# Performance work log

Hardware: AMD Instinct MI355X
Metric: run time of the kernel (lower is better)

## Reference

```python
import jax, jax.numpy as jnp
import numpy as np

DIM = 1024
NUM_HEADS = 16
HEAD_DIM = 64
NUM_LANDMARKS = 256
SEQ_LEN = 4096
BATCH = 4


def setup_inputs() -> dict:
    key = jax.random.key(0)
    ks = jax.random.split(key, 10)
    hd = NUM_HEADS * HEAD_DIM
    s = 1.0 / np.sqrt(DIM)
    inp = {
        "X": jax.random.normal(ks[0], (BATCH, SEQ_LEN, DIM), jnp.float32),
        "mask": jnp.ones((BATCH, SEQ_LEN), jnp.float32),
        "Wq": jax.random.normal(ks[1], (DIM, hd), jnp.float32) * s,
        "bq": jnp.zeros((hd,), jnp.float32),
        "Wk": jax.random.normal(ks[2], (DIM, hd), jnp.float32) * s,
        "bk": jnp.zeros((hd,), jnp.float32),
        "Wv": jax.random.normal(ks[3], (DIM, hd), jnp.float32) * s,
        "bv": jnp.zeros((hd,), jnp.float32),
        "Wff": jax.random.normal(ks[4], (hd, DIM), jnp.float32) * (1.0 / np.sqrt(hd)),
        "bff": jnp.zeros((DIM,), jnp.float32),
    }
    return inp


def _iterative_inv(mat, n_iter=6):
    # mat: [B,H,m,m]; Newton-Schulz style pseudo-inverse, faithful to torch code
    m = mat.shape[-1]
    I = jnp.eye(m, dtype=mat.dtype)
    K = mat
    # global max over the whole tensor, as torch.max with no dim
    denom = jnp.max(jnp.sum(jnp.abs(K), axis=-2)) * jnp.max(jnp.sum(jnp.abs(K), axis=-1))
    V = jnp.swapaxes(K, -1, -2) / denom
    for _ in range(n_iter):
        KV = K @ V
        V = 0.25 * V @ (13.0 * I - KV @ (15.0 * I - KV @ (7.0 * I - KV)))
    return V


def _nystrom_attn(Q, K, V, mask):
    # Q,K,V: [B,H,S,D]; mask: [B,S]
    B, H, S, D = Q.shape
    m = NUM_LANDMARKS
    scale = np.sqrt(np.sqrt(HEAD_DIM)).astype(np.float32)
    Q = Q * mask[:, None, :, None] / scale
    K = K * mask[:, None, :, None] / scale
    Ql = Q.reshape(B, H, m, S // m, D).mean(axis=-2)  # [B,H,m,D]
    Kl = K.reshape(B, H, m, S // m, D).mean(axis=-2)
    k1 = jax.nn.softmax(jnp.einsum('bhsd,bhmd->bhsm', Q, Kl), axis=-1)   # [B,H,S,m]
    k2 = jax.nn.softmax(jnp.einsum('bhmd,bhnd->bhmn', Ql, Kl), axis=-1)  # [B,H,m,m]
    k3 = jax.nn.softmax(
        jnp.einsum('bhmd,bhsd->bhms', Ql, K) - 1e9 * (1.0 - mask[:, None, None, :]),
        axis=-1)  # [B,H,m,S]
    return k1 @ (_iterative_inv(k2) @ (k3 @ V))  # [B,H,S,D]


def reference(X, mask, Wq, bq, Wk, bk, Wv, bv, Wff, bff):
    B, S, _ = X.shape
    def split(t):  # [B,S,H*D] -> [B,H,S,D]
        return t.reshape(B, S, NUM_HEADS, HEAD_DIM).transpose(0, 2, 1, 3)
    Q = split(X @ Wq + bq)
    K = split(X @ Wk + bk)
    V = split(X @ Wv + bv)
    attn = _nystrom_attn(Q, K, V, mask)
    attn = attn.transpose(0, 2, 1, 3).reshape(B, S, NUM_HEADS * HEAD_DIM)
    return attn @ Wff + bff
```

## Files before the change

kernel.cpp:

```cpp
#include <hip/hip_runtime.h>
#include <cstdint>
#include <cstddef>


typedef unsigned short u16;
typedef __attribute__((ext_vector_type(8))) short short8;
typedef __attribute__((ext_vector_type(4))) float f32x4;
typedef __attribute__((ext_vector_type(4))) unsigned short us4;
typedef __attribute__((ext_vector_type(8))) unsigned short us8;

__device__ __forceinline__ float bf2f(u16 u){ return __uint_as_float(((unsigned int)u)<<16); }
__device__ __forceinline__ u16 f2bf(float x){
  unsigned int i = __float_as_uint(x);
  unsigned int r = i + 0x7FFFu + ((i>>16)&1u);
  return (u16)(r>>16);
}
__device__ __forceinline__ f32x4 mfma16(short8 a, short8 b, f32x4 c){
  return __builtin_amdgcn_mfma_f32_16x16x32_bf16(a,b,c,0,0,0);
}
__device__ __forceinline__ void gld16(const void* g, void* l){
  __builtin_amdgcn_global_load_lds(
      (const __attribute__((address_space(1))) unsigned int*)g,
      (__attribute__((address_space(3))) unsigned int*)l, 16, 0, 0);
}

__global__ __launch_bounds__(256) void k2s_k(
    const u16* __restrict__ Ah, const u16* __restrict__ Al,
    const u16* __restrict__ Bh, const u16* __restrict__ Bl,
    float* __restrict__ C)
{
  __shared__ u16 lds[40960];
  const int tid = threadIdx.x;
  const int tileM = blockIdx.x*64;
  const int z = blockIdx.y;
  const int lane = tid&63, wv = tid>>6;
  const int lrow = lane&15, kgrp = lane>>4;
  const u16* baseAh = Ah + (size_t)z*16384 + (size_t)tileM*64;
  const u16* baseAl = Al + (size_t)z*16384 + (size_t)tileM*64;
  const u16* baseBh = Bh + (size_t)z*16384;
  const u16* baseBl = Bl + (size_t)z*16384;

  #pragma unroll
  for (int it=0; it<2; ++it){
    int w = it*256 + tid; int row = w>>3, c = w&7; int cs = c^(row&7);
    gld16(baseAh + (size_t)row*64 + (cs<<3), lds + (w & ~63)*8);
  }
  #pragma unroll
  for (int it=0; it<2; ++it){
    int w = it*256 + tid; int row = w>>3, c = w&7; int cs = c^(row&7);
    gld16(baseAl + (size_t)row*64 + (cs<<3), lds + 4096 + (w & ~63)*8);
  }
  #pragma unroll
  for (int it=0; it<8; ++it){
    int w = it*256 + tid; int row = w>>3, c = w&7; int cs = c^(row&7);
    gld16(baseBh + (size_t)row*64 + (cs<<3), lds + 8192 + (w & ~63)*8);
  }
  #pragma unroll
  for (int it=0; it<8; ++it){
    int w = it*256 + tid; int row = w>>3, c = w&7; int cs = c^(row&7);
    gld16(baseBl + (size_t)row*64 + (cs<<3), lds + 24576 + (w & ~63)*8);
  }
  __syncthreads();

  f32x4 acc[16];
  #pragma unroll
  for (int j=0;j<16;j++) acc[j] = (f32x4){0.f,0.f,0.f,0.f};

  #pragma unroll
  for (int kt=0; kt<2; ++kt){
    int ch = kt*4 + kgrp;
    int ra = wv*16 + lrow;
    short8 ah = *(const short8*)&lds[ra*64 + ((ch^(ra&7))<<3)];
    short8 al = *(const short8*)&lds[4096 + ra*64 + ((ch^(ra&7))<<3)];
    #pragma unroll
    for (int j=0;j<16;j++){
      int rb = j*16 + lrow;
      short8 bh = *(const short8*)&lds[8192 + rb*64 + ((ch^(rb&7))<<3)];
      short8 bl = *(const short8*)&lds[24576 + rb*64 + ((ch^(rb&7))<<3)];
      acc[j] = mfma16(ah, bh, acc[j]);
      acc[j] = mfma16(ah, bl, acc[j]);
      acc[j] = mfma16(al, bh, acc[j]);
    }
  }

  float* Cz = C + (size_t)z*65536;
  #pragma unroll
  for (int r=0;r<4;r++){
    float mx = -3.0e38f;
    #pragma unroll
    for (int j=0;j<16;j++) mx = fmaxf(mx, acc[j][r]);
    #pragma unroll
    for (int d=1; d<16; d<<=1) mx = fmaxf(mx, __shfl_xor(mx, d));
    float p[16]; float ss = 0.f;
    #pragma unroll
    for (int j=0;j<16;j++){ p[j] = expf(acc[j][r]-mx); ss += p[j]; }
    #pragma unroll
    for (int d=1; d<16; d<<=1) ss += __shfl_xor(ss, d);
    float inv = 1.0f/ss;
    int row = tileM + wv*16 + kgrp*4 + r;
    #pragma unroll
    for (int j=0;j<16;j++){
      int col = j*16 + lrow;
      Cz[(size_t)row*256 + col] = p[j]*inv;
    }
  }
}

template<int OUT>
__global__ __launch_bounds__(256) void sgemm_k(
    const u16* __restrict__ Ah, const u16* __restrict__ Al,
    const u16* __restrict__ Bh, const u16* __restrict__ Bl,
    int K, long long sA, long long sB,
    u16* __restrict__ RoH, u16* __restrict__ RoL,
    u16* __restrict__ CoH, u16* __restrict__ CoL,
    float* __restrict__ Fo, long long sO, int ldO,
    float addI, float csgn, float scale,
    const float* __restrict__ bias, const float* __restrict__ ml)
{
  __shared__ u16 lds[16384];
  const int tid = threadIdx.x;
  const int z = blockIdx.z;
  const int tileM = blockIdx.x*64, tileN = blockIdx.y*64;
  const int lane = tid&63, wv = tid>>6;
  const int wr = wv>>1, wc = wv&1;
  const int lrow = lane&15, kgrp = lane>>4;

  const u16* __restrict__ base[4] = {
    Ah + (size_t)z*sA + (size_t)tileM*K,
    Al + (size_t)z*sA + (size_t)tileM*K,
    Bh + (size_t)z*sB + (size_t)tileN*K,
    Bl + (size_t)z*sB + (size_t)tileN*K };

  f32x4 acc[2][2];
  #pragma unroll
  for (int i=0;i<2;i++)
    #pragma unroll
    for (int j=0;j<2;j++) acc[i][j] = (f32x4){0.f,0.f,0.f,0.f};

  for (int k0=0; k0<K; k0+=64){
    #pragma unroll
    for (int t4=0; t4<4; ++t4){
      #pragma unroll
      for (int hf=0; hf<2; ++hf){
        int w = hf*256 + tid;
        int row = w>>3, c = w&7;
        int cs = c ^ (row&7);
        gld16(base[t4] + (size_t)row*K + k0 + cs*8, lds + t4*4096 + (w & ~63)*8);
      }
    }
    __syncthreads();
    #pragma unroll
    for (int kk=0; kk<2; ++kk){
      int ch = kk*4 + kgrp;
      short8 a_h[2], a_l[2], b_h[2], b_l[2];
      #pragma unroll
      for (int i=0;i<2;i++){
        int r = wr*32 + i*16 + lrow;
        int off = r*64 + ((ch ^ (r&7))<<3);
        a_h[i] = *(const short8*)&lds[off];
        a_l[i] = *(const short8*)&lds[4096 + off];
      }
      #pragma unroll
      for (int j=0;j<2;j++){
        int r = wc*32 + j*16 + lrow;
        int off = r*64 + ((ch ^ (r&7))<<3);
        b_h[j] = *(const short8*)&lds[8192 + off];
        b_l[j] = *(const short8*)&lds[12288 + off];
      }
      #pragma unroll
      for (int i=0;i<2;i++)
        #pragma unroll
        for (int j=0;j<2;j++){
          acc[i][j] = mfma16(a_h[i], b_h[j], acc[i][j]);
          acc[i][j] = mfma16(a_h[i], b_l[j], acc[i][j]);
          acc[i][j] = mfma16(a_l[i], b_h[j], acc[i][j]);
        }
    }
    __syncthreads();
  }

  if constexpr (OUT==0 || OUT==1){
    #pragma unroll
    for (int i=0;i<2;i++)
      #pragma unroll
      for (int j=0;j<2;j++){
        int rl0 = wr*32 + i*16 + kgrp*4;
        int cl  = wc*32 + j*16 + lrow;
        #pragma unroll
        for (int q=0;q<4;q++){
          int rl = rl0 + q;
          float p = acc[i][j][q]*scale;
          if constexpr (OUT==0){
            if (RoH){
              u16 h = f2bf(p);
              int lo = rl*64 + (cl ^ ((rl&7)<<3));
              lds[lo] = h;
              lds[4096 + lo] = f2bf(p - bf2f(h));
            }
            float cv = csgn*p + (((tileM+rl)==(tileN+cl))? addI : 0.f);
            u16 ch = f2bf(cv);
            int lo2 = cl*64 + (rl ^ ((cl&7)<<3));
            lds[8192 + lo2] = ch;
            lds[12288 + lo2] = f2bf(cv - bf2f(ch));
          } else {
            lds[cl*64 + (rl ^ ((cl&7)<<3))] = f2bf(p);
          }
        }
      }
    __syncthreads();
    if constexpr (OUT==0){
      if (RoH){
        #pragma unroll
        for (int c2=0;c2<2;c2++){
          int idx = c2*256 + tid;
          int row = idx>>3, seg = idx&7;
          int lo = row*64 + ((seg ^ (row&7))<<3);
          size_t go = (size_t)z*65536 + (size_t)(tileM+row)*256 + tileN + seg*8;
          *(us8*)&RoH[go] = *(const us8*)&lds[lo];
          *(us8*)&RoL[go] = *(const us8*)&lds[4096 + lo];
        }
      }
      #pragma unroll
      for (int c2=0;c2<2;c2++){
        int idx = c2*256 + tid;
        int row = idx>>3, seg = idx&7;
        int lo = row*64 + ((seg ^ (row&7))<<3);
        size_t go = (size_t)z*65536 + (size_t)(tileN+row)*256 + tileM + seg*8;
        *(us8*)&CoH[go] = *(const us8*)&lds[8192 + lo];
        *(us8*)&CoL[go] = *(const us8*)&lds[12288 + lo];
      }
    } else {
      #pragma unroll
      for (int c2=0;c2<2;c2++){
        int idx = c2*256 + tid;
        int row = idx>>3, seg = idx&7;
        int lo = row*64 + ((seg ^ (row&7))<<3);
        *(us8*)&CoH[(size_t)z*16384 + (size_t)(tileN+row)*256 + tileM + seg*8] =
            *(const us8*)&lds[lo];
      }
    }
  } else {
    #pragma unroll
    for (int i=0;i<2;i++)
      #pragma unroll
      for (int j=0;j<2;j++){
        int grow0 = tileM + wr*32 + i*16 + kgrp*4;
        int gcol  = tileN + wc*32 + j*16 + lrow;
        #pragma unroll
        for (int q=0;q<4;q++){
          int grow = grow0+q;
          float v = acc[i][j][q] + ml[grow]*bias[gcol];
          int b = grow>>8, l = grow&255, h = gcol>>6, d = gcol&63;
          size_t oi = (((size_t)(b*16+h)*256 + l)*64 + d);
          Fo[oi] = v;
          if (RoH){
            u16 hh = f2bf(v);
            RoH[oi] = hh;
            RoL[oi] = f2bf(v - bf2f(hh));
          }
        }
      }
  }
}

template<int EPI>
__global__ __launch_bounds__(256) void fgemm_k(
    const u16* __restrict__ A, const u16* __restrict__ Bt, float* __restrict__ Cf,
    u16* __restrict__ Q_, u16* __restrict__ K_, u16* __restrict__ V_,
    int M, int N, int K, int nTilesN,
    const float* __restrict__ bias, const float* __restrict__ rowscale)
{
  __shared__ u16 lds[2*128*64];
  u16* ldsA = lds;
  u16* ldsB = lds + 128*64;

  int flat = blockIdx.y*nTilesN + blockIdx.x;
  int nwg  = gridDim.x*gridDim.y;
  int chunk = nwg >> 3;
  int nid = (flat & 7)*chunk + (flat >> 3);
  int bxM = nid / nTilesN, byN = nid % nTilesN;
  const int tileM = bxM*128, tileN = byN*128;

  const int tid = threadIdx.x;
  const int lane = tid & 63, wv = tid>>6;
  const int wr = wv>>1, wc = wv&1;
  const int lrow = lane&15, kgrp = lane>>4;

  f32x4 acc[4][4];
  #pragma unroll
  for (int i=0;i<4;i++)
    #pragma unroll
    for (int j=0;j<4;j++) acc[i][j] = (f32x4){0.f,0.f,0.f,0.f};

  for (int k0=0; k0<K; k0+=64){
    #pragma unroll
    for (int i=0;i<4;i++){
      int s = i*256 + tid;
      int row = s>>3, c = s&7;
      int cs = c ^ (row&7);
      gld16(A + (size_t)(tileM+row)*K + k0 + cs*8, ldsA + (size_t)(s & ~63)*8);
    }
    #pragma unroll
    for (int i=0;i<4;i++){
      int s = i*256 + tid;
      int row = s>>3, c = s&7;
      int cs = c ^ (row&7);
      gld16(Bt + (size_t)(tileN+row)*K + k0 + cs*8, ldsB + (size_t)(s & ~63)*8);
    }
    __syncthreads();
    #pragma unroll
    for (int kk=0; kk<2; ++kk){
      int ch = kk*4 + kgrp;
      short8 af[4], bf[4];
      #pragma unroll
      for (int i=0;i<4;i++){
        int r = wr*64 + i*16 + lrow;
        af[i] = *(const short8*)&ldsA[r*64 + ((ch^(r&7))<<3)];
      }
      #pragma unroll
      for (int j=0;j<4;j++){
        int r = wc*64 + j*16 + lrow;
        bf[j] = *(const short8*)&ldsB[r*64 + ((ch^(r&7))<<3)];
      }
      #pragma unroll
      for (int i=0;i<4;i++)
        #pragma unroll
        for (int j=0;j<4;j++)
          acc[i][j] = mfma16(af[i], bf[j], acc[i][j]);
    }
    __syncthreads();
  }

  if constexpr (EPI==0){
    #pragma unroll
    for (int i=0;i<4;i++)
      #pragma unroll
      for (int j=0;j<4;j++)
        #pragma unroll
        for (int q=0;q<4;q++){
          int row = tileM + wr*64 + i*16 + kgrp*4 + q;
          int col = tileN + wc*64 + j*16 + lrow;
          Cf[(size_t)row*N + col] = acc[i][j][q] + (bias ? bias[col] : 0.f);
        }
  } else {
    #pragma unroll
    for (int i=0;i<4;i++)
      #pragma unroll
      for (int j=0;j<4;j++)
        #pragma unroll
        for (int q=0;q<4;q++){
          int rloc = wr*64 + i*16 + kgrp*4 + q;
          int cloc = wc*64 + j*16 + lrow;
          int col = tileN + cloc;
          float v = acc[i][j][q] + bias[col];
          if ((col>>10) < 2) v *= rowscale[tileM + rloc];
          lds[rloc*128 + cloc] = f2bf(v);
        }
    __syncthreads();
    #pragma unroll
    for (int c=0;c<8;c++){
      int idx = c*256 + tid;
      int row = idx >> 4;
      int seg = idx & 15;
      int col = tileN + seg*8;
      int which = col >> 10;
      int hd = col & 1023, h = hd>>6, d0 = hd&63;
      int grow = tileM + row;
      int b = grow>>12, s = grow&4095;
      u16* dst = (which==0) ? Q_ : (which==1) ? K_ : V_;
      us8 v = *(const us8*)&lds[row*128 + seg*8];
      *(us8*)&dst[(((size_t)(b*16+h))*4096 + s)*64 + d0] = v;
    }
  }
}

__global__ __launch_bounds__(256) void o3p_k(
    const float* __restrict__ Ql, const u16* __restrict__ Kb, const u16* __restrict__ Vb,
    const float* __restrict__ mask, float* __restrict__ Opart, float* __restrict__ MLpart)
{
  constexpr int QHI=0, QLO=4096, KT=8192, VT=12288, PHI=16640, PLO=20736;
  __shared__ u16 lds[24832];
  const int bx = blockIdx.x, ck = blockIdx.y, z = blockIdx.z;
  const int tid = threadIdx.x;
  const int lane = tid&63, wv = tid>>6;
  const int lrow = lane&15, kgrp = lane>>4;
  const float* Qlz = Ql + (size_t)z*16384 + (size_t)bx*64*64;
  const u16* Kz = Kb + (size_t)z*4096*64;
  const u16* Vz = Vb + (size_t)z*4096*64;
  const float* mrow = mask + (size_t)(z>>4)*4096;

  #pragma unroll
  for (int i=0;i<2;i++){
    int s = i*256 + tid;
    int row = s>>3, c = s&7;
    const float* src = Qlz + row*64 + c*8;
    f32x4 v0 = *(const f32x4*)src;
    f32x4 v1 = *(const f32x4*)(src+4);
    us8 hi, lo;
    #pragma unroll
    for (int e=0;e<4;e++){
      hi[e] = f2bf(v0[e]); lo[e] = f2bf(v0[e]-bf2f(hi[e]));
      hi[4+e] = f2bf(v1[e]); lo[4+e] = f2bf(v1[e]-bf2f(hi[4+e]));
    }
    int ad = row*64 + ((c^(row&7))<<3);
    *(us8*)&lds[QHI+ad] = hi;
    *(us8*)&lds[QLO+ad] = lo;
  }

  float m_r[4], l_r[4];
  f32x4 oacc[4];
  #pragma unroll
  for (int r=0;r<4;r++){ m_r[r] = -3.0e38f; l_r[r] = 0.f; }
  #pragma unroll
  for (int j=0;j<4;j++) oacc[j] = (f32x4){0.f,0.f,0.f,0.f};

  for (int st=0; st<16; ++st){
    int s0 = (ck*16 + st)*64;
    #pragma unroll
    for (int i=0;i<2;i++){
      int s = i*256 + tid;
      int row = s>>3, c = s&7;
      int cs = c ^ (row&7);
      gld16(Kz + (size_t)(s0+row)*64 + cs*8, &lds[KT + (size_t)(s & ~63)*8]);
    }
    #pragma unroll
    for (int i=0;i<2;i++){
      int s = i*256 + tid;
      int row = s>>3, c = s&7;
      us8 v = *(const us8*)(Vz + (size_t)(s0+row)*64 + c*8);
      #pragma unroll
      for (int e=0;e<8;e++) lds[VT + (c*8+e)*68 + row] = v[e];
    }
    __syncthreads();

    f32x4 sacc[4];
    #pragma unroll
    for (int j=0;j<4;j++) sacc[j] = (f32x4){0.f,0.f,0.f,0.f};
    int qr = wv*16 + lrow;
    #pragma unroll
    for (int kk=0; kk<2; ++kk){
      int ch = kk*4 + kgrp;
      short8 ah = *(const short8*)&lds[QHI + qr*64 + ((ch^(qr&7))<<3)];
      short8 alo = *(const short8*)&lds[QLO + qr*64 + ((ch^(qr&7))<<3)];
      #pragma unroll
      for (int j=0;j<4;j++){
        int kr = j*16 + lrow;
        short8 bk = *(const short8*)&lds[KT + kr*64 + ((ch^(kr&7))<<3)];
        sacc[j] = mfma16(ah, bk, sacc[j]);
        sacc[j] = mfma16(alo, bk, sacc[j]);
      }
    }
    float mb[4];
    #pragma unroll
    for (int j=0;j<4;j++) mb[j] = -1.0e9f*(1.0f - mrow[s0 + j*16 + lrow]);
    #pragma unroll
    for (int j=0;j<4;j++)
      #pragma unroll
      for (int r=0;r<4;r++) sacc[j][r] += mb[j];

    #pragma unroll
    for (int r=0;r<4;r++){
      float tm = fmaxf(fmaxf(sacc[0][r],sacc[1][r]), fmaxf(sacc[2][r],sacc[3][r]));
      #pragma unroll
      for (int d=1; d<16; d<<=1) tm = fmaxf(tm, __shfl_xor(tm, d));
      float mn = fmaxf(m_r[r], tm);
      float scf = expf(m_r[r] - mn);
      float ps[4]; float tsum = 0.f;
      #pragma unroll
      for (int j=0;j<4;j++){ ps[j] = expf(sacc[j][r] - mn); tsum += ps[j]; }
      #pragma unroll
      for (int d=1; d<16; d<<=1) tsum += __shfl_xor(tsum, d);
      l_r[r] = l_r[r]*scf + tsum;
      m_r[r] = mn;
      #pragma unroll
      for (int j=0;j<4;j++) oacc[j][r] *= scf;
      int prow = kgrp*4 + r;
      #pragma unroll
      for (int j=0;j<4;j++){
        int key = j*16 + lrow;
        u16 phi = f2bf(ps[j]);
        u16 plo = f2bf(ps[j] - bf2f(phi));
        int ad = wv*1024 + prow*64 + (((key>>3)^(prow&7))<<3) + (key&7);
        lds[PHI+ad] = phi;
        lds[PLO+ad] = plo;
      }
    }

    #pragma unroll
    for (int kk=0; kk<2; ++kk){
      int ch = kk*4 + kgrp;
      int pr = lrow;
      short8 pah = *(const short8*)&lds[PHI + wv*1024 + pr*64 + ((ch^(pr&7))<<3)];
      short8 plo = *(const short8*)&lds[PLO + wv*1024 + pr*64 + ((ch^(pr&7))<<3)];
      #pragma unroll
      for (int j=0;j<4;j++){
        int vr = j*16 + lrow;
        int a0 = VT + vr*68 + ch*8;
        us4 p0 = *(const us4*)&lds[a0];
        us4 p1 = *(const us4*)&lds[a0+4];
        short8 bv_;
        #pragma unroll
        for (int e=0;e<4;e++){ bv_[e] = (short)p0[e]; bv_[4+e] = (short)p1[e]; }
        oacc[j] = mfma16(pah, bv_, oacc[j]);
        oacc[j] = mfma16(plo, bv_, oacc[j]);
      }
    }
    __syncthreads();
  }

  #pragma unroll
  for (int j=0;j<4;j++)
    #pragma unroll
    for (int r=0;r<4;r++){
      int rowl = bx*64 + wv*16 + kgrp*4 + r;
      Opart[(((size_t)(ck*64+z)*256 + rowl)*64) + j*16 + lrow] = oacc[j][r];
    }
  #pragma unroll
  for (int r=0;r<4;r++){
    if (lrow==0){
      int rowl = bx*64 + wv*16 + kgrp*4 + r;
      MLpart[((size_t)(ck*64+z)*256 + rowl)*2 + 0] = m_r[r];
      MLpart[((size_t)(ck*64+z)*256 + rowl)*2 + 1] = l_r[r];
    }
  }
}

__global__ __launch_bounds__(256) void o3c_k(const float* __restrict__ Opart,
    const float* __restrict__ MLpart, u16* __restrict__ O3Th, u16* __restrict__ O3Tl)
{
  int z = blockIdx.x; int t = threadIdx.x;
  float m[4], l[4];
  #pragma unroll
  for (int c=0;c<4;c++){
    m[c] = MLpart[((size_t)(c*64+z)*256 + t)*2 + 0];
    l[c] = MLpart[((size_t)(c*64+z)*256 + t)*2 + 1];
  }
  float M = fmaxf(fmaxf(m[0],m[1]), fmaxf(m[2],m[3]));
  float w[4]; float L = 0.f;
  #pragma unroll
  for (int c=0;c<4;c++){ w[c] = expf(m[c]-M); L += l[c]*w[c]; }
  float inv = 1.0f/L;
  for (int d0=0; d0<16; ++d0){
    f32x4 o = (f32x4){0.f,0.f,0.f,0.f};
    #pragma unroll
    for (int c=0;c<4;c++){
      f32x4 x = *(const f32x4*)(Opart + ((size_t)(c*64+z)*256 + t)*64 + d0*4);
      #pragma unroll
      for (int e=0;e<4;e++) o[e] += w[c]*x[e];
    }
    #pragma unroll
    for (int e=0;e<4;e++){
      float val = o[e]*inv;
      int d = d0*4+e;
      u16 h = f2bf(val);
      O3Th[((size_t)z*64 + d)*256 + t] = h;
      O3Tl[((size_t)z*64 + d)*256 + t] = f2bf(val - bf2f(h));
    }
  }
}

__global__ void fill_k(float* __restrict__ p, int n, float v){
  for (int i = blockIdx.x*256 + threadIdx.x; i < n; i += gridDim.x*256) p[i] = v;
}
__global__ __launch_bounds__(256) void setup_k(
    const float* __restrict__ mask, float* __restrict__ rs,
    const float* __restrict__ bq, const float* __restrict__ bk,
    const float* __restrict__ bv, float* __restrict__ bqkv, float* __restrict__ mx,
    const float* __restrict__ Wq, const float* __restrict__ Wk,
    const float* __restrict__ Wv, const float* __restrict__ Wff,
    u16* __restrict__ Tqkv, u16* __restrict__ Tff,
    u16* __restrict__ QH, u16* __restrict__ QL,
    u16* __restrict__ KH, u16* __restrict__ KL)
{
  __shared__ float t[64][65];
  int b = blockIdx.x;
  if (b < 77){
    if (b < 64){
      int i = b*256 + threadIdx.x;
      rs[i] = mask[i] * 0.3535533905932738f;
    } else if (b < 76){
      int j = (b-64)*256 + threadIdx.x;
      bqkv[j] = (j<1024) ? bq[j] : (j<2048) ? bk[j-1024] : bv[j-2048];
    } else {
      if (threadIdx.x < 2) mx[threadIdx.x] = 0.f;
    }
    return;
  }
  int tt = threadIdx.x; int c = tt&63, r0 = tt>>6;
  if (b < 77+1024){
    int f = b - 77;
    int zi = f >> 8; int r2 = f & 255; int ti = r2 & 15; int tj = r2 >> 4;
    const float* W = (zi==0)?Wq:(zi==1)?Wk:(zi==2)?Wv:Wff;
    u16* T = (zi==3)? Tff : (Tqkv + (size_t)zi*1048576);
    #pragma unroll
    for (int rr=0; rr<16; rr++){
      int r = rr*4 + r0;
      t[r][c] = W[(size_t)(ti*64+r)*1024 + tj*64 + c];
    }
    __syncthreads();
    #pragma unroll
    for (int rr=0; rr<16; rr++){
      int r = rr*4 + r0;
      T[(size_t)(tj*64 + r)*1024 + ti*64 + c] = f2bf(t[c][r]);
    }
  } else {
    int f = b - 77 - 1024;
    int zi = f >> 8; int r2 = f & 255; int ti = r2 & 15; int tj = r2 >> 4;
    const float* W = zi ? Wk : Wq;
    u16* TH = zi ? KH : QH;
    u16* TL = zi ? KL : QL;
    #pragma unroll
    for (int rr=0; rr<16; rr++){
      int r = rr*4 + r0;
      t[r][c] = W[(size_t)(ti*64+r)*1024 + tj*64 + c];
    }
    __syncthreads();
    #pragma unroll
    for (int rr=0; rr<16; rr++){
      int r = rr*4 + r0;
      float v = t[c][r];
      u16 h = f2bf(v);
      TH[(size_t)(tj*64 + r)*1024 + ti*64 + c] = h;
      TL[(size_t)(tj*64 + r)*1024 + ti*64 + c] = f2bf(v - bf2f(h));
    }
  }
}
__global__ __launch_bounds__(256) void pool_k(const float* __restrict__ X, const float* __restrict__ mask,
                                              u16* __restrict__ Xlh, u16* __restrict__ Xll,
                                              float* __restrict__ ml, u16* __restrict__ Xb){
  int bl = blockIdx.x; int b = bl>>8; int l = bl&255;
  const float* Xp = X + ((size_t)b*4096 + (size_t)l*16)*1024;
  const float* mp = mask + (size_t)b*4096 + (size_t)l*16;
  int t = threadIdx.x;
  f32x4 acc = (f32x4){0.f,0.f,0.f,0.f};
  float msum = 0.f;
  #pragma unroll
  for (int j=0;j<16;j++){
    float mj = mp[j];
    msum += mj;
    f32x4 x = *(const f32x4*)(Xp + (size_t)j*1024 + t*4);
    us4 xb;
    #pragma unroll
    for (int c=0;c<4;c++){ acc[c] += mj*x[c]; xb[c] = f2bf(x[c]); }
    *(us4*)(Xb + ((size_t)bl*16 + j)*1024 + t*4) = xb;
  }
  const float c0 = 0.02209708691207961f;
  us4 h, lo;
  #pragma unroll
  for (int c=0;c<4;c++){
    float v = acc[c]*c0;
    h[c] = f2bf(v);
    lo[c] = f2bf(v - bf2f(h[c]));
  }
  *(us4*)(Xlh + (size_t)bl*1024 + t*4) = h;
  *(us4*)(Xll + (size_t)bl*1024 + t*4) = lo;
  if (t==0) ml[bl] = msum * c0;
}
__global__ __launch_bounds__(256) void absmax_k(const float* __restrict__ k2, float* __restrict__ mx){
  int z = blockIdx.x; int t = threadIdx.x;
  const float* A = k2 + (size_t)z*65536;
  float rsum=0.f, csum=0.f;
  for (int j=0;j<256;j++){
    rsum += fabsf(A[t*256+j]);
    csum += fabsf(A[j*256+t]);
  }
  #pragma unroll
  for (int d=1; d<64; d<<=1){
    rsum = fmaxf(rsum, __shfl_xor(rsum, d));
    csum = fmaxf(csum, __shfl_xor(csum, d));
  }
  __shared__ float red[8];
  int wv=t>>6, ln=t&63;
  if (ln==0){ red[wv]=rsum; red[4+wv]=csum; }
  __syncthreads();
  if (t==0){
    float mr = fmaxf(fmaxf(red[0],red[1]),fmaxf(red[2],red[3]));
    float mc = fmaxf(fmaxf(red[4],red[5]),fmaxf(red[6],red[7]));
    atomicMax((int*)&mx[0], __float_as_int(mr));
    atomicMax((int*)&mx[1], __float_as_int(mc));
  }
}
__global__ __launch_bounds__(256) void v0prep_k(const float* __restrict__ K2f, const float* __restrict__ mx,
    u16* __restrict__ K2h, u16* __restrict__ K2l,
    u16* __restrict__ V0rh, u16* __restrict__ V0rl,
    u16* __restrict__ V0ch, u16* __restrict__ V0cl)
{
  int z = blockIdx.y; int bx = blockIdx.x;
  int ti = bx>>2, tj = bx&3;
  __shared__ float tile[64][65];
  const float* A = K2f + (size_t)z*65536;
  int t = threadIdx.x; int c = t&63, r0 = t>>6;
  float invden = 1.0f/(mx[0]*mx[1]);
  #pragma unroll
  for (int rr=0; rr<16; rr++){
    int r = rr*4 + r0;
    float v = A[(size_t)(ti*64 + r)*256 + tj*64 + c];
    tile[r][c] = v;
    size_t idx = (size_t)z*65536 + (size_t)(ti*64+r)*256 + tj*64 + c;
    u16 h = f2bf(v);
    K2h[idx] = h; K2l[idx] = f2bf(v - bf2f(h));
    float w = v*invden;
    h = f2bf(w);
    V0ch[idx] = h; V0cl[idx] = f2bf(w - bf2f(h));
  }
  __syncthreads();
  #pragma unroll
  for (int rr=0; rr<16; rr++){
    int r = rr*4 + r0;
    float w = tile[c][r]*invden;
    size_t idx = (size_t)z*65536 + (size_t)(tj*64+r)*256 + ti*64 + c;
    u16 h = f2bf(w);
    V0rh[idx] = h; V0rl[idx] = f2bf(w - bf2f(h));
  }
}

__device__ __forceinline__ int swz64(int row,int k){
  return row*64 + (((((k>>3)&7) ^ (row&7)))<<3) + (k&7);
}
__device__ __forceinline__ int swz256(int row,int k){
  return row*256 + ((((k>>3) ^ (row&7)))<<3) + (k&7);
}
__global__ __launch_bounds__(256) void attn_k(const u16* __restrict__ Qb,
    const u16* __restrict__ Klb, const u16* __restrict__ tTb,
    u16* __restrict__ attn){
  __shared__ u16 lds[32768];
  const int z = blockIdx.y;
  const int rows0 = blockIdx.x * 64;
  const int tid = threadIdx.x;
  const int lane = tid & 63, wv = tid>>6;
  const int lrow = lane & 15, kgrp = lane>>4;
  const u16* Qz = Qb + ((size_t)z*4096 + rows0)*64;
  const u16* Klz = Klb + (size_t)z*16384;
  const u16* tTz = tTb + (size_t)z*16384;

  #pragma unroll
  for (int i=0;i<8;i++){
    int s = i*256 + tid;
    int row = s>>3, c = s&7;
    gld16(Klz + (size_t)row*64 + ((c^(row&7))<<3), lds + (s & ~63)*8);
  }
  #pragma unroll
  for (int i=0;i<2;i++){
    int s = i*256 + tid;
    int row = s>>3, c = s&7;
    gld16(Qz + (size_t)row*64 + ((c^(row&7))<<3), lds + 16384 + (s & ~63)*8);
  }
  __syncthreads();

  f32x4 acc[4][4];
  #pragma unroll
  for (int i=0;i<4;i++)
    #pragma unroll
    for (int j=0;j<4;j++) acc[i][j] = (f32x4){0.f,0.f,0.f,0.f};
  #pragma unroll
  for (int ks=0; ks<2; ++ks){
    int ko = ks*32 + kgrp*8;
    short8 a[4], b[4];
    #pragma unroll
    for (int i=0;i<4;i++) a[i] = *(const short8*)&lds[16384 + swz64(16*i+lrow, ko)];
    #pragma unroll
    for (int j=0;j<4;j++) b[j] = *(const short8*)&lds[swz64(wv*64 + j*16 + lrow, ko)];
    #pragma unroll
    for (int i=0;i<4;i++)
      #pragma unroll
      for (int j=0;j<4;j++) acc[i][j] = mfma16(a[i], b[j], acc[i][j]);
  }
  __syncthreads();

  #pragma unroll
  for (int i=0;i<8;i++){
    int s = i*256 + tid;
    int row = s>>5, c = s&31;
    int gch = (c & ~7) | ((c ^ row) & 7);
    gld16(tTz + (size_t)row*256 + (gch<<3), lds + 16384 + (s & ~63)*8);
  }

  float* r0 = (float*)lds;
  float* r1 = r0 + 256;
  #pragma unroll
  for (int i=0;i<4;i++)
    #pragma unroll
    for (int r=0;r<4;r++){
      float mx = fmaxf(fmaxf(acc[i][0][r], acc[i][1][r]), fmaxf(acc[i][2][r], acc[i][3][r]));
      #pragma unroll
      for (int d=1; d<16; d<<=1) mx = fmaxf(mx, __shfl_xor(mx, d));
      if (lrow==0) r0[(16*i + kgrp*4 + r)*4 + wv] = mx;
    }
  __syncthreads();
  float inv_ir[4][4];
  #pragma unroll
  for (int i=0;i<4;i++)
    #pragma unroll
    for (int r=0;r<4;r++){
      int row = 16*i + kgrp*4 + r;
      float gm = fmaxf(fmaxf(r0[row*4+0], r0[row*4+1]), fmaxf(r0[row*4+2], r0[row*4+3]));
      float s = 0.f;
      #pragma unroll
      for (int j=0;j<4;j++){
        acc[i][j][r] = expf(acc[i][j][r] - gm);
        s += acc[i][j][r];
      }
      #pragma unroll
      for (int d=1; d<16; d<<=1) s += __shfl_xor(s, d);
      if (lrow==0) r1[row*4 + wv] = s;
      inv_ir[i][r] = 0.f; (void)inv_ir;
    }
  __syncthreads();
  #pragma unroll
  for (int i=0;i<4;i++)
    #pragma unroll
    for (int r=0;r<4;r++){
      int row = 16*i + kgrp*4 + r;
      inv_ir[i][r] = 1.0f/(r1[row*4+0]+r1[row*4+1]+r1[row*4+2]+r1[row*4+3]);
    }
  __syncthreads();

  #pragma unroll
  for (int i=0;i<4;i++)
    #pragma unroll
    for (int j=0;j<4;j++)
      #pragma unroll
      for (int r=0;r<4;r++){
        int row = 16*i + kgrp*4 + r;
        int l = wv*64 + j*16 + lrow;
        lds[swz256(row, l)] = f2bf(acc[i][j][r]*inv_ir[i][r]);
      }
  __syncthreads();

  f32x4 o[4];
  #pragma unroll
  for (int j=0;j<4;j++) o[j] = (f32x4){0.f,0.f,0.f,0.f};
  #pragma unroll
  for (int ks=0; ks<8; ++ks){
    int ko = ks*32 + kgrp*8;
    short8 a = *(const short8*)&lds[swz256(16*wv + lrow, ko)];
    #pragma unroll
    for (int j=0;j<4;j++){
      short8 bb = *(const short8*)&lds[16384 + swz256(j*16 + lrow, ko)];
      o[j] = mfma16(a, bb, o[j]);
    }
  }
  __syncthreads();
  #pragma unroll
  for (int j=0;j<4;j++)
    #pragma unroll
    for (int r=0;r<4;r++){
      int m = 16*wv + kgrp*4 + r;
      lds[m*64 + j*16 + lrow] = f2bf(o[j][r]);
    }
  __syncthreads();
  int b = z>>4, h = z&15;
  #pragma unroll
  for (int c=0;c<2;c++){
    int idx = c*256 + tid;
    int row = idx >> 3;
    int seg = idx & 7;
    us8 v = *(const us8*)&lds[row*64 + seg*8];
    *(us8*)&attn[((size_t)b*4096 + rows0 + row)*1024 + (size_t)h*64 + seg*8] = v;
  }
}

extern "C" void kernel_launch(void* const* d_in, const int* in_sizes, int n_in,
                              void* d_out, int out_size, void* d_ws, size_t ws_size,
                              hipStream_t stream) {
  (void)in_sizes; (void)n_in;
  const float* X    = (const float*)d_in[0];
  const float* mask = (const float*)d_in[1];
  const float* Wq   = (const float*)d_in[2];
  const float* bq   = (const float*)d_in[3];
  const float* Wk   = (const float*)d_in[4];
  const float* bk   = (const float*)d_in[5];
  const float* Wv   = (const float*)d_in[6];
  const float* bv   = (const float*)d_in[7];
  const float* Wff  = (const float*)d_in[8];
  const float* bff  = (const float*)d_in[9];
  float* outp = (float*)d_out;
  char* ws = (char*)d_ws;

  auto MiB = [](size_t x){ return x<<20; };
  const size_t O_QB   = 0;
  const size_t O_KB   = MiB(32);
  const size_t O_VB   = MiB(64);
  const size_t O_XB   = MiB(96);
  const size_t O_RG[4][2] = {
    {MiB(32),MiB(40)}, {MiB(48),MiB(56)}, {MiB(64),MiB(72)}, {MiB(80),MiB(88)} };
  const size_t O_QLH  = MiB(96),  O_QLL = MiB(98), O_KLL = MiB(100);
  const size_t O_OPART= MiB(96);
  const size_t O_MLP  = MiB(112);
  const size_t O_XAH  = MiB(96),  O_XAL = MiB(104);
  const size_t O_K2H  = MiB(112), O_K2L = MiB(120);
  const size_t O_K2F  = MiB(128);
  const size_t O_WQKVT= MiB(128);
  const size_t O_XLH  = MiB(134), O_XLL = MiB(136);
  const size_t O_WQTH = MiB(138), O_WQTL = MiB(140);
  const size_t O_QL   = MiB(144);
  const size_t O_TTB  = MiB(144);
  const size_t O_KL   = MiB(148);
  const size_t O_O3TH = MiB(152), O_O3TL = MiB(154);
  const size_t O_WKTH = MiB(152), O_WKTL = MiB(154);
  const size_t O_WFFT = MiB(156);
  const size_t O_KLB  = MiB(158);
  const size_t O_ATTN = MiB(32);
  const size_t O_RS   = MiB(162);
  const size_t O_ML   = O_RS + 65536;
  const size_t O_MX   = O_ML + 4096;
  const size_t O_BQKV = O_MX + 256;
  const size_t NEED   = O_BQKV + 16384;

  if (ws_size < NEED){
    fill_k<<<2048,256,0,stream>>>(outp, out_size, 1.0e9f);
    return;
  }

  u16*   Qb   = (u16*)(ws + O_QB);
  u16*   Kb   = (u16*)(ws + O_KB);
  u16*   Vb   = (u16*)(ws + O_VB);
  u16*   Xb   = (u16*)(ws + O_XB);
  u16*   WqkvT= (u16*)(ws + O_WQKVT);
  u16*   WffT = (u16*)(ws + O_WFFT);
  float* bqkv = (float*)(ws + O_BQKV);
  float* Ql   = (float*)(ws + O_QL);
  float* Kl   = (float*)(ws + O_KL);
  u16*   QlH  = (u16*)(ws + O_QLH);
  u16*   QlL  = (u16*)(ws + O_QLL);
  u16*   KlL  = (u16*)(ws + O_KLL);
  u16*   Klb  = (u16*)(ws + O_KLB);
  u16*   tTb  = (u16*)(ws + O_TTB);
  float* K2f  = (float*)(ws + O_K2F);
  float* rs   = (float*)(ws + O_RS);
  float* ml   = (float*)(ws + O_ML);
  float* Mx   = (float*)(ws + O_MX);
  float* Opart= (float*)(ws + O_OPART);
  float* MLp  = (float*)(ws + O_MLP);
  u16*   O3Th = (u16*)(ws + O_O3TH);
  u16*   O3Tl = (u16*)(ws + O_O3TL);
  u16*   K2h  = (u16*)(ws + O_K2H);
  u16*   K2l  = (u16*)(ws + O_K2L);
  u16*   XAh  = (u16*)(ws + O_XAH);
  u16*   XAl  = (u16*)(ws + O_XAL);
  u16*   Xlh  = (u16*)(ws + O_XLH);
  u16*   Xll  = (u16*)(ws + O_XLL);
  u16*   WqTh = (u16*)(ws + O_WQTH);
  u16*   WqTl = (u16*)(ws + O_WQTL);
  u16*   WkTh = (u16*)(ws + O_WKTH);
  u16*   WkTl = (u16*)(ws + O_WKTL);
  u16*   AttnB= (u16*)(ws + O_ATTN);
  u16* RGH[4]; u16* RGL[4];
  for (int i=0;i<4;i++){ RGH[i] = (u16*)(ws + O_RG[i][0]); RGL[i] = (u16*)(ws + O_RG[i][1]); }

  setup_k<<<1613,256,0,stream>>>(mask, rs, bq, bk, bv, bqkv, Mx,
      Wq, Wk, Wv, Wff, WqkvT, WffT, WqTh, WqTl, WkTh, WkTl);
  pool_k<<<1024,256,0,stream>>>(X, mask, Xlh, Xll, ml, Xb);

  fgemm_k<1><<<dim3(24,128),256,0,stream>>>(Xb, WqkvT, nullptr, Qb, Kb, Vb,
      16384, 3072, 1024, 24, bqkv, rs);

  sgemm_k<2><<<dim3(16,16,1),256,0,stream>>>(Xlh, Xll, WqTh, WqTl, 1024, 0, 0,
      QlH, QlL, nullptr, nullptr, Ql, 0, 0, 0.f, 0.f, 1.f, bq, ml);
  sgemm_k<2><<<dim3(16,16,1),256,0,stream>>>(Xlh, Xll, WkTh, WkTl, 1024, 0, 0,
      Klb, KlL, nullptr, nullptr, Kl, 0, 0, 0.f, 0.f, 1.f, bk, ml);

  k2s_k<<<dim3(4,64),256,0,stream>>>(QlH, QlL, Klb, KlL, K2f);

  o3p_k<<<dim3(4,4,64),256,0,stream>>>(Ql, Kb, Vb, mask, Opart, MLp);
  o3c_k<<<64,256,0,stream>>>(Opart, MLp, O3Th, O3Tl);

  absmax_k<<<64,256,0,stream>>>(K2f, Mx);
  v0prep_k<<<dim3(16,64),256,0,stream>>>(K2f, Mx, K2h, K2l, RGH[1], RGL[1], RGH[0], RGL[0]);
  int vc=0, vr=1, kv=2, x2=3;
  for (int it=0; it<6; ++it){
    sgemm_k<0><<<dim3(4,4,64),256,0,stream>>>(K2h, K2l, RGH[vc], RGL[vc], 256, 65536, 65536,
        RGH[kv], RGL[kv], XAh, XAl, nullptr, 0, 0, 7.f, -1.f, 1.f, nullptr, nullptr);
    sgemm_k<0><<<dim3(4,4,64),256,0,stream>>>(RGH[kv], RGL[kv], XAh, XAl, 256, 65536, 65536,
        nullptr, nullptr, RGH[x2], RGL[x2], nullptr, 0, 0, 15.f, -1.f, 1.f, nullptr, nullptr);
    sgemm_k<0><<<dim3(4,4,64),256,0,stream>>>(RGH[kv], RGL[kv], RGH[x2], RGL[x2], 256, 65536, 65536,
        nullptr, nullptr, XAh, XAl, nullptr, 0, 0, 13.f, -1.f, 1.f, nullptr, nullptr);
    sgemm_k<0><<<dim3(4,4,64),256,0,stream>>>(RGH[vr], RGL[vr], XAh, XAl, 256, 65536, 65536,
        RGH[kv], RGL[kv], RGH[x2], RGL[x2], nullptr, 0, 0, 0.f, 1.f, 0.25f, nullptr, nullptr);
    int nvc=x2, nvr=kv, nkv=vc, nx2=vr;
    vc=nvc; vr=nvr; kv=nkv; x2=nx2;
  }
  sgemm_k<1><<<dim3(4,1,64),256,0,stream>>>(RGH[vr], RGL[vr], O3Th, O3Tl, 256, 65536, 16384,
      nullptr,nullptr, tTb, nullptr, nullptr, 0, 0, 0.f, 0.f, 1.f, nullptr, nullptr);

  attn_k<<<dim3(64,64),256,0,stream>>>(Qb, Klb, tTb, AttnB);

  fgemm_k<0><<<dim3(8,128),256,0,stream>>>(AttnB, WffT, outp, nullptr, nullptr, nullptr,
      16384, 1024, 1024, 8, bff, nullptr);
}
```

Measured before the change: 1.114 ms.

## Use 8-wave fgemm blocks and merge pooling and absmax into other launches

The dense GEMM kernel now runs 512 threads per 128x128 tile instead of 256. Each of the 8 waves covers a 64x32 sub-tile, so per-thread accumulators halve and more waves are available to hide latency. The X pooling and bf16 conversion moves into extra blocks of the setup kernel, and the K2 absmax reduction merges into the O3 combine kernel, removing two launches. The cost is less per-wave fragment reuse (af loads are now shared across only 2 B fragments) and some branch divergence between block roles in the merged kernels.

Result: faster. 1.018 ms (median of 2 runs) (-8.6%).

```diff
diff --git a/kernel.cpp b/kernel.cpp
--- a/kernel.cpp
+++ b/kernel.cpp
@@ -264,7 +264,7 @@
 }
 
 template<int EPI>
-__global__ __launch_bounds__(256) void fgemm_k(
+__global__ __launch_bounds__(512) void fgemm_k(
     const u16* __restrict__ A, const u16* __restrict__ Bt, float* __restrict__ Cf,
     u16* __restrict__ Q_, u16* __restrict__ K_, u16* __restrict__ V_,
     int M, int N, int K, int nTilesN,
@@ -283,26 +283,26 @@
 
   const int tid = threadIdx.x;
   const int lane = tid & 63, wv = tid>>6;
-  const int wr = wv>>1, wc = wv&1;
+  const int wr = wv>>2, wc = wv&3;
   const int lrow = lane&15, kgrp = lane>>4;
 
-  f32x4 acc[4][4];
+  f32x4 acc[4][2];
   #pragma unroll
   for (int i=0;i<4;i++)
     #pragma unroll
-    for (int j=0;j<4;j++) acc[i][j] = (f32x4){0.f,0.f,0.f,0.f};
+    for (int j=0;j<2;j++) acc[i][j] = (f32x4){0.f,0.f,0.f,0.f};
 
   for (int k0=0; k0<K; k0+=64){
     #pragma unroll
-    for (int i=0;i<4;i++){
-      int s = i*256 + tid;
+    for (int i=0;i<2;i++){
+      int s = i*512 + tid;
       int row = s>>3, c = s&7;
       int cs = c ^ (row&7);
       gld16(A + (size_t)(tileM+row)*K + k0 + cs*8, ldsA + (size_t)(s & ~63)*8);
     }
     #pragma unroll
-    for (int i=0;i<4;i++){
-      int s = i*256 + tid;
+    for (int i=0;i<2;i++){
+      int s = i*512 + tid;
       int row = s>>3, c = s&7;
       int cs = c ^ (row&7);
       gld16(Bt + (size_t)(tileN+row)*K + k0 + cs*8, ldsB + (size_t)(s & ~63)*8);
@@ -311,21 +311,21 @@
     #pragma unroll
     for (int kk=0; kk<2; ++kk){
       int ch = kk*4 + kgrp;
-      short8 af[4], bf[4];
+      short8 af[4], bf[2];
       #pragma unroll
       for (int i=0;i<4;i++){
         int r = wr*64 + i*16 + lrow;
         af[i] = *(const short8*)&ldsA[r*64 + ((ch^(r&7))<<3)];
       }
       #pragma unroll
-      for (int j=0;j<4;j++){
-        int r = wc*64 + j*16 + lrow;
+      for (int j=0;j<2;j++){
+        int r = wc*32 + j*16 + lrow;
         bf[j] = *(const short8*)&ldsB[r*64 + ((ch^(r&7))<<3)];
       }
       #pragma unroll
       for (int i=0;i<4;i++)
         #pragma unroll
-        for (int j=0;j<4;j++)
+        for (int j=0;j<2;j++)
           acc[i][j] = mfma16(af[i], bf[j], acc[i][j]);
     }
     __syncthreads();
@@ -335,22 +335,22 @@
     #pragma unroll
     for (int i=0;i<4;i++)
       #pragma unroll
-      for (int j=0;j<4;j++)
+      for (int j=0;j<2;j++)
         #pragma unroll
         for (int q=0;q<4;q++){
           int row = tileM + wr*64 + i*16 + kgrp*4 + q;
-          int col = tileN + wc*64 + j*16 + lrow;
+          int col = tileN + wc*32 + j*16 + lrow;
           Cf[(size_t)row*N + col] = acc[i][j][q] + (bias ? bias[col] : 0.f);
         }
   } else {
     #pragma unroll
     for (int i=0;i<4;i++)
       #pragma unroll
-      for (int j=0;j<4;j++)
+      for (int j=0;j<2;j++)
         #pragma unroll
         for (int q=0;q<4;q++){
           int rloc = wr*64 + i*16 + kgrp*4 + q;
-          int cloc = wc*64 + j*16 + lrow;
+          int cloc = wc*32 + j*16 + lrow;
           int col = tileN + cloc;
           float v = acc[i][j][q] + bias[col];
           if ((col>>10) < 2) v *= rowscale[tileM + rloc];
@@ -358,8 +358,8 @@
         }
     __syncthreads();
     #pragma unroll
-    for (int c=0;c<8;c++){
-      int idx = c*256 + tid;
+    for (int c=0;c<4;c++){
+      int idx = c*512 + tid;
       int row = idx >> 4;
       int seg = idx & 15;
       int col = tileN + seg*8;
@@ -525,36 +525,63 @@
   }
 }
 
-__global__ __launch_bounds__(256) void o3c_k(const float* __restrict__ Opart,
-    const float* __restrict__ MLpart, u16* __restrict__ O3Th, u16* __restrict__ O3Tl)
+__global__ __launch_bounds__(256) void o3cab_k(const float* __restrict__ Opart,
+    const float* __restrict__ MLpart, u16* __restrict__ O3Th, u16* __restrict__ O3Tl,
+    const float* __restrict__ k2, float* __restrict__ mx)
 {
-  int z = blockIdx.x; int t = threadIdx.x;
-  float m[4], l[4];
-  #pragma unroll
-  for (int c=0;c<4;c++){
-    m[c] = MLpart[((size_t)(c*64+z)*256 + t)*2 + 0];
-    l[c] = MLpart[((size_t)(c*64+z)*256 + t)*2 + 1];
-  }
-  float M = fmaxf(fmaxf(m[0],m[1]), fmaxf(m[2],m[3]));
-  float w[4]; float L = 0.f;
-  #pragma unroll
-  for (int c=0;c<4;c++){ w[c] = expf(m[c]-M); L += l[c]*w[c]; }
-  float inv = 1.0f/L;
-  for (int d0=0; d0<16; ++d0){
-    f32x4 o = (f32x4){0.f,0.f,0.f,0.f};
+  int t = threadIdx.x;
+  if (blockIdx.x < 64){
+    int z = blockIdx.x;
+    float m[4], l[4];
     #pragma unroll
     for (int c=0;c<4;c++){
-      f32x4 x = *(const f32x4*)(Opart + ((size_t)(c*64+z)*256 + t)*64 + d0*4);
-      #pragma unroll
-      for (int e=0;e<4;e++) o[e] += w[c]*x[e];
-    }
-    #pragma unroll
-    for (int e=0;e<4;e++){
-      float val = o[e]*inv;
-      int d = d0*4+e;
-      u16 h = f2bf(val);
-      O3Th[((size_t)z*64 + d)*256 + t] = h;
-      O3Tl[((size_t)z*64 + d)*256 + t] = f2bf(val - bf2f(h));
+      m[c] = MLpart[((size_t)(c*64+z)*256 + t)*2 + 0];
+      l[c] = MLpart[((size_t)(c*64+z)*256 + t)*2 + 1];
+    }
+    float M = fmaxf(fmaxf(m[0],m[1]), fmaxf(m[2],m[3]));
+    float w[4]; float L = 0.f;
+    #pragma unroll
+    for (int c=0;c<4;c++){ w[c] = expf(m[c]-M); L += l[c]*w[c]; }
+    float inv = 1.0f/L;
+    for (int d0=0; d0<16; ++d0){
+      f32x4 o = (f32x4){0.f,0.f,0.f,0.f};
+      #pragma unroll
+      for (int c=0;c<4;c++){
+        f32x4 x = *(const f32x4*)(Opart + ((size_t)(c*64+z)*256 + t)*64 + d0*4);
+        #pragma unroll
+        for (int e=0;e<4;e++) o[e] += w[c]*x[e];
+      }
+      #pragma unroll
+      for (int e=0;e<4;e++){
+        float val = o[e]*inv;
+        int d = d0*4+e;
+        u16 h = f2bf(val);
+        O3Th[((size_t)z*64 + d)*256 + t] = h;
+        O3Tl[((size_t)z*64 + d)*256 + t] = f2bf(val - bf2f(h));
+      }
+    }
+  } else {
+    int z = blockIdx.x - 64;
+    const float* A = k2 + (size_t)z*65536;
+    float rsum=0.f, csum=0.f;
+    for (int j=0;j<256;j++){
+      rsum += fabsf(A[t*256+j]);
+      csum += fabsf(A[j*256+t]);
+    }
+    #pragma unroll
+    for (int d=1; d<64; d<<=1){
+      rsum = fmaxf(rsum, __shfl_xor(rsum, d));
+      csum = fmaxf(csum, __shfl_xor(csum, d));
+    }
+    __shared__ float red[8];
+    int wv=t>>6, ln=t&63;
+    if (ln==0){ red[wv]=rsum; red[4+wv]=csum; }
+    __syncthreads();
+    if (t==0){
+      float mr = fmaxf(fmaxf(red[0],red[1]),fmaxf(red[2],red[3]));
+      float mc = fmaxf(fmaxf(red[4],red[5]),fmaxf(red[6],red[7]));
+      atomicMax((int*)&mx[0], __float_as_int(mr));
+      atomicMax((int*)&mx[1], __float_as_int(mc));
     }
   }
 }
@@ -570,7 +597,10 @@
     const float* __restrict__ Wv, const float* __restrict__ Wff,
     u16* __restrict__ Tqkv, u16* __restrict__ Tff,
     u16* __restrict__ QH, u16* __restrict__ QL,
-    u16* __restrict__ KH, u16* __restrict__ KL)
+    u16* __restrict__ KH, u16* __restrict__ KL,
+    const float* __restrict__ X,
+    u16* __restrict__ Xlh, u16* __restrict__ Xll,
+    float* __restrict__ ml, u16* __restrict__ Xb)
 {
   __shared__ float t[64][65];
   int b = blockIdx.x;
@@ -586,6 +616,36 @@
     }
     return;
   }
+  if (b >= 1613){
+    int bl = b - 1613; int bb = bl>>8; int l = bl&255;
+    const float* Xp = X + ((size_t)bb*4096 + (size_t)l*16)*1024;
+    const float* mp = mask + (size_t)bb*4096 + (size_t)l*16;
+    int tt = threadIdx.x;
+    f32x4 acc = (f32x4){0.f,0.f,0.f,0.f};
+    float msum = 0.f;
+    #pragma unroll
+    for (int j=0;j<16;j++){
+      float mj = mp[j];
+      msum += mj;
+      f32x4 x = *(const f32x4*)(Xp + (size_t)j*1024 + tt*4);
+      us4 xb;
+      #pragma unroll
+      for (int c=0;c<4;c++){ acc[c] += mj*x[c]; xb[c] = f2bf(x[c]); }
+      *(us4*)(Xb + ((size_t)bl*16 + j)*1024 + tt*4) = xb;
+    }
+    const float c0 = 0.02209708691207961f;
+    us4 h, lo;
+    #pragma unroll
+    for (int c=0;c<4;c++){
+      float v = acc[c]*c0;
+      h[c] = f2bf(v);
+      lo[c] = f2bf(v - bf2f(h[c]));
+    }
+    *(us4*)(Xlh + (size_t)bl*1024 + tt*4) = h;
+    *(us4*)(Xll + (size_t)bl*1024 + tt*4) = lo;
+    if (tt==0) ml[bl] = msum * c0;
+    return;
+  }
   int tt = threadIdx.x; int c = tt&63, r0 = tt>>6;
   if (b < 77+1024){
     int f = b - 77;
@@ -623,61 +683,6 @@
       TH[(size_t)(tj*64 + r)*1024 + ti*64 + c] = h;
       TL[(size_t)(tj*64 + r)*1024 + ti*64 + c] = f2bf(v - bf2f(h));
     }
-  }
-}
-__global__ __launch_bounds__(256) void pool_k(const float* __restrict__ X, const float* __restrict__ mask,
-                                              u16* __restrict__ Xlh, u16* __restrict__ Xll,
-                                              float* __restrict__ ml, u16* __restrict__ Xb){
-  int bl = blockIdx.x; int b = bl>>8; int l = bl&255;
-  const float* Xp = X + ((size_t)b*4096 + (size_t)l*16)*1024;
-  const float* mp = mask + (size_t)b*4096 + (size_t)l*16;
-  int t = threadIdx.x;
-  f32x4 acc = (f32x4){0.f,0.f,0.f,0.f};
-  float msum = 0.f;
-  #pragma unroll
-  for (int j=0;j<16;j++){
-    float mj = mp[j];
-    msum += mj;
-    f32x4 x = *(const f32x4*)(Xp + (size_t)j*1024 + t*4);
-    us4 xb;
-    #pragma unroll
-    for (int c=0;c<4;c++){ acc[c] += mj*x[c]; xb[c] = f2bf(x[c]); }
-    *(us4*)(Xb + ((size_t)bl*16 + j)*1024 + t*4) = xb;
-  }
-  const float c0 = 0.02209708691207961f;
-  us4 h, lo;
-  #pragma unroll
-  for (int c=0;c<4;c++){
-    float v = acc[c]*c0;
-    h[c] = f2bf(v);
-    lo[c] = f2bf(v - bf2f(h[c]));
-  }
-  *(us4*)(Xlh + (size_t)bl*1024 + t*4) = h;
-  *(us4*)(Xll + (size_t)bl*1024 + t*4) = lo;
-  if (t==0) ml[bl] = msum * c0;
-}
-__global__ __launch_bounds__(256) void absmax_k(const float* __restrict__ k2, float* __restrict__ mx){
-  int z = blockIdx.x; int t = threadIdx.x;
-  const float* A = k2 + (size_t)z*65536;
-  float rsum=0.f, csum=0.f;
-  for (int j=0;j<256;j++){
-    rsum += fabsf(A[t*256+j]);
-    csum += fabsf(A[j*256+t]);
-  }
-  #pragma unroll
-  for (int d=1; d<64; d<<=1){
-    rsum = fmaxf(rsum, __shfl_xor(rsum, d));
-    csum = fmaxf(csum, __shfl_xor(csum, d));
-  }
-  __shared__ float red[8];
-  int wv=t>>6, ln=t&63;
-  if (ln==0){ red[wv]=rsum; red[4+wv]=csum; }
-  __syncthreads();
-  if (t==0){
-    float mr = fmaxf(fmaxf(red[0],red[1]),fmaxf(red[2],red[3]));
-    float mc = fmaxf(fmaxf(red[4],red[5]),fmaxf(red[6],red[7]));
-    atomicMax((int*)&mx[0], __float_as_int(mr));
-    atomicMax((int*)&mx[1], __float_as_int(mc));
   }
 }
 __global__ __launch_bounds__(256) void v0prep_k(const float* __restrict__ K2f, const float* __restrict__ mx,
@@ -948,11 +953,11 @@
   u16* RGH[4]; u16* RGL[4];
   for (int i=0;i<4;i++){ RGH[i] = (u16*)(ws + O_RG[i][0]); RGL[i] = (u16*)(ws + O_RG[i][1]); }
 
-  setup_k<<<1613,256,0,stream>>>(mask, rs, bq, bk, bv, bqkv, Mx,
-      Wq, Wk, Wv, Wff, WqkvT, WffT, WqTh, WqTl, WkTh, WkTl);
-  pool_k<<<1024,256,0,stream>>>(X, mask, Xlh, Xll, ml, Xb);
-
-  fgemm_k<1><<<dim3(24,128),256,0,stream>>>(Xb, WqkvT, nullptr, Qb, Kb, Vb,
+  setup_k<<<2637,256,0,stream>>>(mask, rs, bq, bk, bv, bqkv, Mx,
+      Wq, Wk, Wv, Wff, WqkvT, WffT, WqTh, WqTl, WkTh, WkTl,
+      X, Xlh, Xll, ml, Xb);
+
+  fgemm_k<1><<<dim3(24,128),512,0,stream>>>(Xb, WqkvT, nullptr, Qb, Kb, Vb,
       16384, 3072, 1024, 24, bqkv, rs);
 
   sgemm_k<2><<<dim3(16,16,1),256,0,stream>>>(Xlh, Xll, WqTh, WqTl, 1024, 0, 0,
@@ -963,9 +968,8 @@
   k2s_k<<<dim3(4,64),256,0,stream>>>(QlH, QlL, Klb, KlL, K2f);
 
   o3p_k<<<dim3(4,4,64),256,0,stream>>>(Ql, Kb, Vb, mask, Opart, MLp);
-  o3c_k<<<64,256,0,stream>>>(Opart, MLp, O3Th, O3Tl);
-
-  absmax_k<<<64,256,0,stream>>>(K2f, Mx);
+  o3cab_k<<<128,256,0,stream>>>(Opart, MLp, O3Th, O3Tl, K2f, Mx);
+
   v0prep_k<<<dim3(16,64),256,0,stream>>>(K2f, Mx, K2h, K2l, RGH[1], RGL[1], RGH[0], RGL[0]);
   int vc=0, vr=1, kv=2, x2=3;
   for (int it=0; it<6; ++it){
@@ -985,6 +989,6 @@
 
   attn_k<<<dim3(64,64),256,0,stream>>>(Qb, Klb, tTb, AttnB);
 
-  fgemm_k<0><<<dim3(8,128),256,0,stream>>>(AttnB, WffT, outp, nullptr, nullptr, nullptr,
+  fgemm_k<0><<<dim3(8,128),512,0,stream>>>(AttnB, WffT, outp, nullptr, nullptr, nullptr,
       16384, 1024, 1024, 8, bff, nullptr);
 }
```
